# Kernel tuning notes

Hardware: AMD Instinct MI355X
Metric: run time of the kernel (lower is better)

## Reference

```python
import math
import jax, jax.numpy as jnp
import numpy as np

B, T, D = 4, 1024, 1024
H = 16
HD = D // H       # head_dim
DE = 64           # d_event
NT = 8            # n_event_types
NR = 64           # n_rules
NH = 4            # n_hits
NA = 2            # n_alternatives
SQ = math.sqrt(HD)


def setup_inputs() -> dict:
    key = jax.random.key(0)
    ks = jax.random.split(key, 16)
    s = 0.02
    f = jnp.float32
    return {
        "x": jax.random.normal(ks[0], (B, T, D), f),
        "W_node": jax.random.normal(ks[1], (D, D), f) * s,
        "W_value": jax.random.normal(ks[2], (D, D), f) * s,
        "W_out": jax.random.normal(ks[3], (D, D), f) * s,
        "arity_w": jax.random.normal(ks[4], (H, HD), f) * s,   # arity=3 -> one extra axis weight
        "W_event": jax.random.normal(ks[5], (D, DE), f) * s,
        "W_type": jax.random.normal(ks[6], (D, NT), f) * s,
        "patterns": jax.random.normal(ks[7], (NR, DE), f) * s,
        "W_actions": jax.random.normal(ks[8], (NA, D, D), f) * s,
        "W_alt": jax.random.normal(ks[9], (DE, NA), f) * s,
        "log_temp": jnp.zeros((), f),
        "Wg1": jax.random.normal(ks[10], (2 * D + 1, D), f) * s,
        "bg1": jnp.zeros((D,), f),
        "Wg2": jax.random.normal(ks[11], (D, 1), f) * s,
        "bg2": jnp.zeros((1,), f),
    }


def reference(x, W_node, W_value, W_out, arity_w, W_event, W_type, patterns,
              W_actions, W_alt, log_temp, Wg1, bg1, Wg2, bg2):
    # --- IsotropicAttention (arity=3, eval mode so dropout is identity) ---
    nodes = (x @ W_node).reshape(B, T, H, HD).transpose(0, 2, 1, 3)    # (B,H,T,HD)
    values = (x @ W_value).reshape(B, T, H, HD).transpose(0, 2, 1, 3)  # (B,H,T,HD)
    scores = jnp.einsum('bhtd,bhsd->bhts', nodes, nodes)
    scores = (scores + scores.transpose(0, 1, 3, 2)) * (0.5 / SQ)      # symmetrize + scale
    ax = jnp.einsum('bhtd,hd->bht', nodes, arity_w)                    # ternary axis score
    mod = jax.nn.sigmoid((ax[:, :, :, None] + ax[:, :, None, :]) / SQ)
    scores = scores * mod
    attn = jax.nn.softmax(scores, axis=-1)
    attn_out = jnp.einsum('bhts,bhsd->bthd', attn, values).reshape(B, T, D) @ W_out
    x1 = x + attn_out
    # --- EventGenerator ---
    events = x1 @ W_event                                              # (B,T,DE)
    event_types = jax.nn.softmax(x1 @ W_type, axis=-1)                 # (B,T,NT)
    # --- RuleBank: soft top-k hit activation ---
    en = events / jnp.maximum(jnp.linalg.norm(events, axis=-1, keepdims=True), 1e-12)
    pn = patterns / jnp.maximum(jnp.linalg.norm(patterns, axis=-1, keepdims=True), 1e-12)
    sim = en @ pn.T                                                    # (B,T,NR)
    topk_vals, topk_idx = jax.lax.top_k(sim, NH)
    temp = jnp.clip(jnp.exp(log_temp), 0.01, 10.0)
    hit_w = jax.nn.softmax(topk_vals / temp, axis=-1)                  # (B,T,NH)
    hit_patterns = patterns[topk_idx]                                  # (B,T,NH,DE)
    weighted_pattern = jnp.einsum('btkd,btk->btd', hit_patterns, hit_w)
    alt_w = jax.nn.softmax((weighted_pattern @ W_alt) / temp, axis=-1) # (B,T,NA)
    acted = jnp.einsum('btd,ade->btae', x1, W_actions)                 # (B,T,NA,D)
    actions_out = jnp.einsum('btae,bta->bte', acted, alt_w)
    hit_strength = jnp.max(topk_vals, axis=-1, keepdims=True)
    actions_out = actions_out * jax.nn.sigmoid(hit_strength)
    # --- TransactionGate: soft commit/rollback ---
    entropy = -jnp.sum(event_types * jnp.log(event_types + 1e-10), axis=-1, keepdims=True)
    entropy_norm = entropy / math.log(NT)
    gin = jnp.concatenate([x1, actions_out, entropy_norm], axis=-1)    # (B,T,2D+1)
    g = jax.nn.sigmoid(jax.nn.silu(gin @ Wg1 + bg1) @ Wg2 + bg2)       # (B,T,1)
    return x1 + g * actions_out
```

## Files before the change

kernel.cpp:

```cpp
#include <hip/hip_runtime.h>
#include <hip/hip_bf16.h>
#include <math.h>

#define B_  4
#define T_  1024
#define D_  1024
#define H_  16
#define HD_ 64
#define DE_ 64
#define NT_ 8
#define NR_ 64
#define NH_ 4

typedef __attribute__((ext_vector_type(8))) short short8;
typedef __attribute__((ext_vector_type(4))) short short4v;
typedef __attribute__((ext_vector_type(2))) unsigned uint2v;
typedef __attribute__((ext_vector_type(4))) float f4;

typedef __attribute__((address_space(1))) const unsigned int guint;
typedef __attribute__((address_space(3))) unsigned int suint;

__device__ __forceinline__ short f2bf(float f) {
    unsigned x = __float_as_uint(f);
    unsigned r = (x + 0x7fffu + ((x >> 16) & 1u)) >> 16;
    return (short)r;
}
__device__ __forceinline__ float bf2f(short s) {
    return __uint_as_float(((unsigned)(unsigned short)s) << 16);
}

__device__ __forceinline__ int swz64(int row, int slot) {
    return row * 64 + ((slot ^ (row & 7)) << 3);
}

__global__ __launch_bounds__(256) void castx_k(
    const float* __restrict__ x, short* __restrict__ xb)
{
    size_t i = ((size_t)blockIdx.x * 256 + threadIdx.x) * 8;
    float4 v0 = *(const float4*)&x[i];
    float4 v1 = *(const float4*)&x[i + 4];
    short8 o;
    o[0] = f2bf(v0.x); o[1] = f2bf(v0.y); o[2] = f2bf(v0.z); o[3] = f2bf(v0.w);
    o[4] = f2bf(v1.x); o[5] = f2bf(v1.y); o[6] = f2bf(v1.z); o[7] = f2bf(v1.w);
    *(short8*)&xb[i] = o;
}

struct TJ { const float* src; short* dst; int K, N, rs, ro, base; };
struct TJobs { TJ j[7]; };

__global__ __launch_bounds__(256) void tcast_all(TJobs jb)
{
    int bid = blockIdx.x;
    int ji = 0;
#pragma unroll
    for (int i = 1; i < 7; i++) if (bid >= jb.j[i].base) ji = i;
    const float* src = jb.j[ji].src;
    short* dst = jb.j[ji].dst;
    const int K = jb.j[ji].K, N = jb.j[ji].N;
    const int rs = jb.j[ji].rs, ro = jb.j[ji].ro;
    int rel = bid - jb.j[ji].base;
    int tiles_n = N >> 6;
    int k0 = (rel / tiles_n) * 64, n0 = (rel % tiles_n) * 64;

    __shared__ float tile[64][65];
    const int tid = threadIdx.x;
    const int r = tid >> 4, c = (tid & 15) * 4;
#pragma unroll
    for (int rep = 0; rep < 4; rep++) {
        int rr = rep * 16 + r;
        float4 v = *(const float4*)&src[(size_t)(k0 + rr) * N + n0 + c];
        tile[rr][c] = v.x; tile[rr][c + 1] = v.y; tile[rr][c + 2] = v.z; tile[rr][c + 3] = v.w;
    }
    __syncthreads();
#pragma unroll
    for (int rep = 0; rep < 4; rep++) {
        int n = rep * 16 + r;
        short4v p;
        p[0] = f2bf(tile[c + 0][n]);
        p[1] = f2bf(tile[c + 1][n]);
        p[2] = f2bf(tile[c + 2][n]);
        p[3] = f2bf(tile[c + 3][n]);
        *(short4v*)&dst[(size_t)((n0 + n) * rs + ro) * K + k0 + c] = p;
    }
}

__global__ __launch_bounds__(256) void ttype_k(
    const float* __restrict__ Wt, short* __restrict__ BTe)
{
    int idx = blockIdx.x * 256 + threadIdx.x;
    int n = idx >> 10, k = idx & 1023;
    BTe[(size_t)(64 + n) * 1024 + k] = f2bf(Wt[k * 8 + n]);
}

template<int AM>
__global__ __launch_bounds__(256) void gemm4(
    const short* __restrict__ A1, const short* __restrict__ A2, int Ks,
    const short* __restrict__ BT,
    float* __restrict__ C, short* __restrict__ Cb1, short* __restrict__ Cb2,
    int M, int N, int K, int epi,
    const float* __restrict__ resid, const float* __restrict__ ent,
    const float* __restrict__ w1e, const float* __restrict__ bias,
    const float* __restrict__ altw, const float* __restrict__ hitsig)
{
    constexpr int BM = AM * 32;
    constexpr int AR = (AM == 4) ? 2 : 4;
    constexpr int ANV = 64 / AR / 8;
    __shared__ short As[BM * 72];
    __shared__ short Bs[128 * 72];
    const int tid = threadIdx.x, wave = tid >> 6, lane = tid & 63;
    const int lrow = lane & 15, lq = lane >> 4;
    int bid = blockIdx.x;
    int tiles_m = M / BM;
    int mpx = tiles_m >> 3;
    int xcd = bid & 7, idx = bid >> 3;
    int mt = xcd * mpx + (idx % mpx);
    int nt = idx / mpx;
    const int m0 = mt * BM, n0 = nt * 128;
    const int wm = (wave >> 1) * (AM * 16), wn = (wave & 1) * 64;
    const int K2 = K - Ks;
    const int arow = tid / AR, ash = (tid % AR) * (64 / AR);
    const int brow = tid >> 1, bsh = (tid & 1) * 32;

    short8 va[ANV], vb[4];
    auto loadA = [&](int k0) {
        int ka = k0 + ash;
        const short* ap = (ka < Ks)
            ? A1 + (size_t)(m0 + arow) * Ks + ka
            : A2 + (size_t)(m0 + arow) * K2 + (ka - Ks);
#pragma unroll
        for (int u = 0; u < ANV; u++) va[u] = *(const short8*)(ap + u * 8);
    };
    auto loadB = [&](int k0) {
        const short* bp = BT + (size_t)(n0 + brow) * K + k0 + bsh;
#pragma unroll
        for (int u = 0; u < 4; u++) vb[u] = *(const short8*)(bp + u * 8);
    };

    loadA(0); loadB(0);
    f4 acc[AM][4] = {};

    for (int k0 = 0; k0 < K; k0 += 64) {
        __syncthreads();
#pragma unroll
        for (int u = 0; u < ANV; u++)
            *(short8*)&As[arow * 72 + ash + u * 8] = va[u];
#pragma unroll
        for (int u = 0; u < 4; u++)
            *(short8*)&Bs[brow * 72 + bsh + u * 8] = vb[u];
        __syncthreads();
        if (k0 + 64 < K) { loadA(k0 + 64); loadB(k0 + 64); }
#pragma unroll
        for (int kh = 0; kh < 2; kh++) {
            short8 af[AM], bfv[4];
#pragma unroll
            for (int i = 0; i < AM; i++)
                af[i] = *(short8*)&As[(wm + i * 16 + lrow) * 72 + kh * 32 + lq * 8];
#pragma unroll
            for (int j = 0; j < 4; j++)
                bfv[j] = *(short8*)&Bs[(wn + j * 16 + lrow) * 72 + kh * 32 + lq * 8];
#pragma unroll
            for (int i = 0; i < AM; i++)
#pragma unroll
                for (int j = 0; j < 4; j++)
                    acc[i][j] = __builtin_amdgcn_mfma_f32_16x16x32_bf16(
                        af[i], bfv[j], acc[i][j], 0, 0, 0);
        }
    }

#pragma unroll
    for (int i = 0; i < AM; i++) {
#pragma unroll
        for (int r = 0; r < 4; r++) {
            int row = m0 + wm + i * 16 + lq * 4 + r;
            float w0 = 0.f, w1 = 0.f, hs = 0.f;
            if (epi == 5) { w0 = altw[row * 2]; w1 = altw[row * 2 + 1]; hs = hitsig[row]; }
#pragma unroll
            for (int j = 0; j < 4; j++) {
                int col = n0 + wn + j * 16 + lrow;
                float v = acc[i][j][r];
                if (epi == 0) {
                    C[(size_t)row * N + col] = v;
                } else if (epi == 1) {
                    v += resid[(size_t)row * N + col];
                    C[(size_t)row * N + col] = v;
                    Cb1[(size_t)row * N + col] = f2bf(v);
                } else if (epi == 2) {
                    if (col < 1024) Cb1[(size_t)row * 1024 + col] = f2bf(v);
                    else            Cb2[(size_t)row * 1024 + col - 1024] = f2bf(v);
                } else if (epi == 3) {
                    v += ent[row] * w1e[col] + bias[col];
                    float sv = v * __builtin_amdgcn_rcpf(1.f + __expf(-v));
                    Cb1[(size_t)row * N + col] = f2bf(sv);
                } else {
                    float other = __shfl_xor(v, 1);
                    if ((lane & 1) == 0) {
                        float cv = (w0 * v + w1 * other) * hs;
                        Cb1[(size_t)row * 1024 + (col >> 1)] = f2bf(cv);
                    }
                }
            }
        }
    }
}

template<int AM>
__global__ __launch_bounds__(256) void gemm7(
    const short* __restrict__ A1, const short* __restrict__ A2, int Ks,
    const short* __restrict__ BT,
    float* __restrict__ C, short* __restrict__ Cb1, short* __restrict__ Cb2,
    int M, int N, int K, int epi,
    const float* __restrict__ resid, const float* __restrict__ ent,
    const float* __restrict__ w1e, const float* __restrict__ bias,
    const float* __restrict__ altw, const float* __restrict__ hitsig)
{
    constexpr int BM = AM * 32;
    constexpr int AISS = BM / 32;
    __shared__ short As[2][BM * 64];
    __shared__ short Bs[2][128 * 64];
    const int tid = threadIdx.x, wave = tid >> 6, lane = tid & 63;
    const int lrow = lane & 15, lq = lane >> 4;
    int bid = blockIdx.x;
    int tiles_m = M / BM;
    int mpx = tiles_m >> 3;
    int xcd = bid & 7, idx = bid >> 3;
    int mt = xcd * mpx + (idx % mpx);
    int ntile = idx / mpx;
    const int m0 = mt * BM, n0 = ntile * 128;
    const int wm = (wave >> 1) * (AM * 16), wn = (wave & 1) * 64;
    const int K2 = K - Ks;

    const int l8 = lane >> 3;
    const int cs = ((lane & 7) ^ l8) << 3;

    auto stageA = [&](int k0, int bu) {
#pragma unroll
        for (int u = 0; u < AISS; u++) {
            int r = wave * (AISS * 8) + u * 8 + l8;
            int ka = k0 + cs;
            const short* gp = (ka < Ks)
                ? A1 + (size_t)(m0 + r) * Ks + ka
                : A2 + (size_t)(m0 + r) * K2 + (ka - Ks);
            short* lp = &As[bu][wave * (AISS * 512) + u * 512];
            __builtin_amdgcn_global_load_lds((guint*)gp, (suint*)lp, 16, 0, 0);
        }
    };
    auto stageB = [&](int k0, int bu) {
#pragma unroll
        for (int u = 0; u < 4; u++) {
            int r = wave * 32 + u * 8 + l8;
            const short* gp = BT + (size_t)(n0 + r) * K + k0 + cs;
            short* lp = &Bs[bu][wave * 2048 + u * 512];
            __builtin_amdgcn_global_load_lds((guint*)gp, (suint*)lp, 16, 0, 0);
        }
    };

    stageA(0, 0); stageB(0, 0);
    f4 acc[AM][4] = {};
    const int nsteps = K >> 6;

    for (int t = 0; t < nsteps; t++) {
        const int cur = t & 1;
        __syncthreads();
        if (t + 1 < nsteps) {
            stageA((t + 1) << 6, cur ^ 1);
            stageB((t + 1) << 6, cur ^ 1);
        }
#pragma unroll
        for (int kh = 0; kh < 2; kh++) {
            short8 af[AM], bfv[4];
#pragma unroll
            for (int i = 0; i < AM; i++)
                af[i] = *(short8*)&As[cur][swz64(wm + i * 16 + lrow, kh * 4 + lq)];
#pragma unroll
            for (int j = 0; j < 4; j++)
                bfv[j] = *(short8*)&Bs[cur][swz64(wn + j * 16 + lrow, kh * 4 + lq)];
#pragma unroll
            for (int i = 0; i < AM; i++)
#pragma unroll
                for (int j = 0; j < 4; j++)
                    acc[i][j] = __builtin_amdgcn_mfma_f32_16x16x32_bf16(
                        af[i], bfv[j], acc[i][j], 0, 0, 0);
        }
    }

#pragma unroll
    for (int i = 0; i < AM; i++) {
#pragma unroll
        for (int r = 0; r < 4; r++) {
            int row = m0 + wm + i * 16 + lq * 4 + r;
            float w0 = 0.f, w1 = 0.f, hs = 0.f;
            if (epi == 5) { w0 = altw[row * 2]; w1 = altw[row * 2 + 1]; hs = hitsig[row]; }
#pragma unroll
            for (int j = 0; j < 4; j++) {
                int col = n0 + wn + j * 16 + lrow;
                float v = acc[i][j][r];
                if (epi == 0) {
                    C[(size_t)row * N + col] = v;
                } else if (epi == 1) {
                    v += resid[(size_t)row * N + col];
                    C[(size_t)row * N + col] = v;
                    Cb1[(size_t)row * N + col] = f2bf(v);
                } else if (epi == 2) {
                    if (col < 1024) Cb1[(size_t)row * 1024 + col] = f2bf(v);
                    else            Cb2[(size_t)row * 1024 + col - 1024] = f2bf(v);
                } else if (epi == 3) {
                    v += ent[row] * w1e[col] + bias[col];
                    float sv = v * __builtin_amdgcn_rcpf(1.f + __expf(-v));
                    Cb1[(size_t)row * N + col] = f2bf(sv);
                } else {
                    float other = __shfl_xor(v, 1);
                    if ((lane & 1) == 0) {
                        float cv = (w0 * v + w1 * other) * hs;
                        Cb1[(size_t)row * 1024 + (col >> 1)] = f2bf(cv);
                    }
                }
            }
        }
    }
}

__global__ __launch_bounds__(256) void vtrans_k(
    const short* __restrict__ vb, short* __restrict__ vtg)
{
    const int b = blockIdx.z, h = blockIdx.y, t0 = blockIdx.x * 64;
    const int tid = threadIdx.x;
    __shared__ short tile[64 * 72];
    const int row = tid >> 2, c = (tid & 3) * 16;
    const short* p = vb + (size_t)(b * T_ + t0 + row) * D_ + h * 64 + c;
    *(short8*)&tile[row * 72 + c + 0] = *(const short8*)(p + 0);
    *(short8*)&tile[row * 72 + c + 8] = *(const short8*)(p + 8);
    __syncthreads();
    short8 o0, o1;
#pragma unroll
    for (int i = 0; i < 8; i++) o0[i] = tile[(c + i) * 72 + row];
#pragma unroll
    for (int i = 0; i < 8; i++) o1[i] = tile[(c + 8 + i) * 72 + row];
    short* q = vtg + (size_t)((b * H_ + h) * 64 + row) * T_ + t0 + c;
    *(short8*)(q + 0) = o0;
    *(short8*)(q + 8) = o1;
}

__global__ __launch_bounds__(256) void ax_k(
    const short* __restrict__ nodes_bf, const float* __restrict__ arity_w,
    float* __restrict__ ax)
{
    int idx = blockIdx.x * 256 + threadIdx.x;
    int t = idx & (T_ - 1);
    int h = (idx >> 10) & (H_ - 1);
    int b = idx >> 14;
    const short* np_ = nodes_bf + (((size_t)b * T_ + t) * H_ + h) * HD_;
    float s = 0.f;
#pragma unroll
    for (int d = 0; d < HD_; d += 8) {
        short8 n8 = *(const short8*)&np_[d];
#pragma unroll
        for (int q = 0; q < 8; q++) s += bf2f(n8[q]) * arity_w[h * HD_ + d + q];
    }
    ax[idx] = s;
}

__global__ __launch_bounds__(256) void attn8_k(
    const short* __restrict__ nodes_bf, const short* __restrict__ vtg,
    const float* __restrict__ ax, short* __restrict__ attnp)
{
    const int b = blockIdx.z, h = blockIdx.y, t0 = blockIdx.x * 64;
    const int tid = threadIdx.x;
    const int wave = tid >> 6, lane = tid & 63;
    const int lrow = lane & 15, lq = lane >> 4;
    const int wm = wave * 16;
    const int row = tid >> 2, c4 = tid & 3;

    __shared__ short Ns[64 * 64];
    __shared__ short Vt[64 * 64];
    __shared__ short Pm[64 * 64];

    const short* qp = nodes_bf + (size_t)(b * T_ + t0 + wm + lrow) * D_ + h * 64;
    const short8 bt0 = *(const short8*)(qp + lq * 8);
    const short8 bt1 = *(const short8*)(qp + 32 + lq * 8);
    const float at8 = ax[(size_t)(b * H_ + h) * T_ + t0 + wm + lrow] * 0.125f;

    const short* np0 = nodes_bf + (size_t)(b * T_ + row) * D_ + h * 64 + c4 * 16;
    const short* vp0 = vtg + (size_t)((b * H_ + h) * 64 + row) * T_ + c4 * 16;
    const float* axp_ = ax + (size_t)(b * H_ + h) * T_;

    short8 vn0, vn1, vv0, vv1;
    f4 axv[4];
    auto preload = [&](int s0) {
        const short* np = np0 + (size_t)s0 * D_;
        const short* vp = vp0 + s0;
        vn0 = *(const short8*)(np + 0);
        vn1 = *(const short8*)(np + 8);
        vv0 = *(const short8*)(vp + 0);
        vv1 = *(const short8*)(vp + 8);
#pragma unroll
        for (int j = 0; j < 4; j++)
            axv[j] = *(const f4*)&axp_[s0 + j * 16 + lq * 4];
    };

    preload(0);

    float l_reg = 0.f;
    f4 O[4] = {};
    f4 axc[4];

    for (int s0 = 0; s0 < T_; s0 += 64) {
        __syncthreads();
        *(short8*)&Ns[swz64(row, 2 * c4 + 0)] = vn0;
        *(short8*)&Ns[swz64(row, 2 * c4 + 1)] = vn1;
        *(short8*)&Vt[swz64(row, 2 * c4 + 0)] = vv0;
        *(short8*)&Vt[swz64(row, 2 * c4 + 1)] = vv1;
#pragma unroll
        for (int j = 0; j < 4; j++) axc[j] = axv[j];
        __syncthreads();
        if (s0 + 64 < T_) preload(s0 + 64);

        float psum = 0.f;
#pragma unroll
        for (int j = 0; j < 4; j++) {
            short8 a0 = *(short8*)&Ns[swz64(j * 16 + lrow, lq)];
            short8 a1 = *(short8*)&Ns[swz64(j * 16 + lrow, 4 + lq)];
            f4 s = {0.f, 0.f, 0.f, 0.f};
            s = __builtin_amdgcn_mfma_f32_16x16x32_bf16(a0, bt0, s, 0, 0, 0);
            s = __builtin_amdgcn_mfma_f32_16x16x32_bf16(a1, bt1, s, 0, 0, 0);
            float p0, p1, p2, p3;
            {
                float z, zz, t1, mK;
                z = fmaf(axc[j][0], 0.125f, at8); zz = z * z;
                t1 = fmaf(zz, -0.0037570183f, 0.04508422f);
                mK = fmaf(z, t1, 0.09016844f);
                p0 = __builtin_amdgcn_exp2f(s[0] * mK);
                z = fmaf(axc[j][1], 0.125f, at8); zz = z * z;
                t1 = fmaf(zz, -0.0037570183f, 0.04508422f);
                mK = fmaf(z, t1, 0.09016844f);
                p1 = __builtin_amdgcn_exp2f(s[1] * mK);
                z = fmaf(axc[j][2], 0.125f, at8); zz = z * z;
                t1 = fmaf(zz, -0.0037570183f, 0.04508422f);
                mK = fmaf(z, t1, 0.09016844f);
                p2 = __builtin_amdgcn_exp2f(s[2] * mK);
                z = fmaf(axc[j][3], 0.125f, at8); zz = z * z;
                t1 = fmaf(zz, -0.0037570183f, 0.04508422f);
                mK = fmaf(z, t1, 0.09016844f);
                p3 = __builtin_amdgcn_exp2f(s[3] * mK);
            }
            psum += (p0 + p1) + (p2 + p3);
            unsigned u0, u1;
            asm("v_cvt_pk_bf16_f32 %0, %1, %2" : "=v"(u0) : "v"(p0), "v"(p1));
            asm("v_cvt_pk_bf16_f32 %0, %1, %2" : "=v"(u1) : "v"(p2), "v"(p3));
            uint2v uu; uu[0] = u0; uu[1] = u1;
            *(uint2v*)&Pm[swz64(wm + lrow, 2 * j + (lq >> 1)) + (lq & 1) * 4] = uu;
        }
        l_reg += psum;

        short8 pa0 = *(short8*)&Pm[swz64(wm + lrow, lq)];
        short8 pa1 = *(short8*)&Pm[swz64(wm + lrow, 4 + lq)];
#pragma unroll
        for (int dj = 0; dj < 4; dj++) {
            short8 v0 = *(short8*)&Vt[swz64(dj * 16 + lrow, lq)];
            short8 v1 = *(short8*)&Vt[swz64(dj * 16 + lrow, 4 + lq)];
            O[dj] = __builtin_amdgcn_mfma_f32_16x16x32_bf16(pa0, v0, O[dj], 0, 0, 0);
            O[dj] = __builtin_amdgcn_mfma_f32_16x16x32_bf16(pa1, v1, O[dj], 0, 0, 0);
        }
    }

    l_reg += __shfl_xor(l_reg, 16);
    l_reg += __shfl_xor(l_reg, 32);

    float linv[4];
#pragma unroll
    for (int r = 0; r < 4; r++)
        linv[r] = __builtin_amdgcn_rcpf(__shfl(l_reg, lq * 4 + r));
#pragma unroll
    for (int dj = 0; dj < 4; dj++)
#pragma unroll
        for (int r = 0; r < 4; r++)
            attnp[(size_t)(b * T_ + t0 + wm + lq * 4 + r) * D_ + h * 64 + dj * 16 + lrow] =
                f2bf(O[dj][r] * linv[r]);
}

__global__ __launch_bounds__(64) void pnorm_k(
    const float* __restrict__ patterns, float* __restrict__ pn)
{
    int r = blockIdx.x, lane = threadIdx.x;
    float v = patterns[r * 64 + lane];
    float ss = v * v;
    for (int off = 1; off < 64; off <<= 1) ss += __shfl_xor(ss, off);
    pn[r * 64 + lane] = v / fmaxf(sqrtf(ss), 1e-12f);
}

__global__ __launch_bounds__(256) void token2_k(
    const float* __restrict__ evlg, const float* __restrict__ pn,
    const float* __restrict__ patterns, const float* __restrict__ W_alt,
    const float* __restrict__ log_temp,
    float* __restrict__ entn, float* __restrict__ altw, float* __restrict__ hitsig)
{
    const int tid = threadIdx.x, wave = tid >> 6, lane = tid & 63;
    __shared__ float pn_sh[64 * 68];
    __shared__ float pat_sh[64 * 68];
    __shared__ float en_sh[4][68];
    {
        int row = tid >> 2, c = (tid & 3) * 16;
#pragma unroll
        for (int u = 0; u < 4; u++) {
            *(float4*)&pn_sh[row * 68 + c + u * 4]  = *(const float4*)&pn[row * 64 + c + u * 4];
            *(float4*)&pat_sh[row * 68 + c + u * 4] = *(const float4*)&patterns[row * 64 + c + u * 4];
        }
    }
    float temp = expf(log_temp[0]);
    temp = fminf(fmaxf(temp, 0.01f), 10.f);
    const float tinv = 1.f / temp;
    __syncthreads();

#pragma unroll
    for (int rep = 0; rep < 2; rep++) {
        const int m = blockIdx.x * 8 + wave * 2 + rep;
        float ev = evlg[(size_t)m * 128 + lane];
        float ss = ev * ev;
        for (int off = 1; off < 64; off <<= 1) ss += __shfl_xor(ss, off);
        float en = ev * __builtin_amdgcn_rcpf(fmaxf(sqrtf(ss), 1e-12f));
        en_sh[wave][lane] = en;
        float entv;
        {
            float lgt = evlg[(size_t)m * 128 + 64 + (lane & 7)];
            float mx = lgt;
            for (int off = 1; off < 8; off <<= 1) mx = fmaxf(mx, __shfl_xor(mx, off));
            float p = __expf(lgt - mx);
            float sum = p;
            for (int off = 1; off < 8; off <<= 1) sum += __shfl_xor(sum, off);
            float pi = p / sum;
            float term = -pi * __logf(pi + 1e-10f);
            float e = term;
            for (int off = 1; off < 8; off <<= 1) e += __shfl_xor(e, off);
            entv = e * 0.4808983f;
        }
        float sim = 0.f;
#pragma unroll
        for (int u = 0; u < 16; u++) {
            float4 e4 = *(float4*)&en_sh[wave][u * 4];
            float4 p4 = *(float4*)&pn_sh[lane * 68 + u * 4];
            sim += e4.x * p4.x + e4.y * p4.y + e4.z * p4.z + e4.w * p4.w;
        }
        float v = sim;
        float tv[NH_]; int tix[NH_];
#pragma unroll
        for (int kk = 0; kk < NH_; kk++) {
            float mv = v; int mi = lane;
            if (v == -1e30f) mi = 127;
            for (int off = 1; off < 64; off <<= 1) {
                float ov = __shfl_xor(mv, off);
                int   oi = __shfl_xor(mi, off);
                if (ov > mv || (ov == mv && oi < mi)) { mv = ov; mi = oi; }
            }
            tv[kk] = mv; tix[kk] = mi;
            if (lane == mi) v = -1e30f;
        }
        float hmx = tv[0];
        float hw[NH_], hsum = 0.f;
#pragma unroll
        for (int kk = 0; kk < NH_; kk++) { hw[kk] = __expf((tv[kk] - hmx) * tinv); hsum += hw[kk]; }
        float hsr = __builtin_amdgcn_rcpf(hsum);
        float wp = 0.f;
#pragma unroll
        for (int kk = 0; kk < NH_; kk++) wp += hw[kk] * hsr * pat_sh[tix[kk] * 68 + lane];
        float a0 = wp * W_alt[lane * 2 + 0];
        float a1 = wp * W_alt[lane * 2 + 1];
        for (int off = 1; off < 64; off <<= 1) {
            a0 += __shfl_xor(a0, off);
            a1 += __shfl_xor(a1, off);
        }
        a0 *= tinv; a1 *= tinv;
        float amx = fmaxf(a0, a1);
        float e0 = __expf(a0 - amx), e1 = __expf(a1 - amx);
        if (lane == 0) {
            float zr = __builtin_amdgcn_rcpf(e0 + e1);
            altw[m * 2 + 0] = e0 * zr;
            altw[m * 2 + 1] = e1 * zr;
            hitsig[m] = __builtin_amdgcn_rcpf(1.f + __expf(-tv[0]));
            entn[m] = entv;
        }
    }
}

__global__ __launch_bounds__(256) void gate_k(
    const short* __restrict__ h1_bf, const float* __restrict__ Wg2,
    const float* __restrict__ bg2, const float* __restrict__ x1,
    const short* __restrict__ actions_bf, float* __restrict__ out)
{
    const int m = blockIdx.x, tid = threadIdx.x;
    float part = 0.f;
    for (int d = tid; d < D_; d += 256)
        part += bf2f(h1_bf[(size_t)m * D_ + d]) * Wg2[d];
    __shared__ float red[256];
    red[tid] = part;
    __syncthreads();
    for (int w = 128; w > 0; w >>= 1) {
        if (tid < w) red[tid] += red[tid + w];
        __syncthreads();
    }
    float g = 1.f / (1.f + expf(-(red[0] + bg2[0])));
    for (int d = tid; d < D_; d += 256) {
        size_t i = (size_t)m * D_ + d;
        out[i] = x1[i] + g * bf2f(actions_bf[i]);
    }
}

extern "C" void kernel_launch(void* const* d_in, const int* in_sizes, int n_in,
                              void* d_out, int out_size, void* d_ws, size_t ws_size,
                              hipStream_t stream)
{
    const float* x        = (const float*)d_in[0];
    const float* W_node   = (const float*)d_in[1];
    const float* W_value  = (const float*)d_in[2];
    const float* W_out    = (const float*)d_in[3];
    const float* arity_w  = (const float*)d_in[4];
    const float* W_event  = (const float*)d_in[5];
    const float* W_type   = (const float*)d_in[6];
    const float* patterns = (const float*)d_in[7];
    const float* W_act    = (const float*)d_in[8];
    const float* W_alt    = (const float*)d_in[9];
    const float* log_temp = (const float*)d_in[10];
    const float* Wg1      = (const float*)d_in[11];
    const float* bg1      = (const float*)d_in[12];
    const float* Wg2      = (const float*)d_in[13];
    const float* bg2      = (const float*)d_in[14];
    float* out = (float*)d_out;

    const int M = B_ * T_;
    float* x1     = (float*)d_ws;
    float* evlg   = x1 + 4194304;
    float* axp    = evlg + 524288;
    float* pn     = axp + 65536;
    float* entn   = pn + 4096;
    float* altw   = entn + 4096;
    float* hitsig = altw + 8192;
    short* big       = (short*)(hitsig + 4096);
    short* xbf       = big;
    short* nodes_bf  = big + 1 * 4194304;
    short* values_bf = big + 2 * 4194304;
    short* vtg       = big + 3 * 4194304;
    short* x1_bf     = big + 4 * 4194304;
    short* wts       = big + 5 * 4194304;
    short* WnvT  = wts;
    short* WoT   = wts + 2 * 1048576;
    short* WaT   = wts + 3 * 1048576;
    short* Wg1T  = wts + 5 * 1048576;
    short* BTe   = wts + 7 * 1048576;
    short* actions_bf = vtg;
    short* h1_bf      = xbf;

    dim3 blk(256);
    dim3 g_bh(T_ / 64, H_, B_);

    castx_k<<<2048, blk, 0, stream>>>(x, xbf);
    pnorm_k<<<NR_, 64, 0, stream>>>(patterns, pn);
    TJobs jb;
    jb.j[0] = {W_node,            WnvT,           1024, 1024, 1, 0,    0};
    jb.j[1] = {W_value,           WnvT + 1048576, 1024, 1024, 1, 0,  256};
    jb.j[2] = {W_out,             WoT,            1024, 1024, 1, 0,  512};
    jb.j[3] = {W_act,             WaT,            1024, 1024, 2, 0,  768};
    jb.j[4] = {W_act + 1048576,   WaT,            1024, 1024, 2, 1, 1024};
    jb.j[5] = {Wg1,               Wg1T,           2048, 1024, 1, 0, 1280};
    jb.j[6] = {W_event,           BTe,            1024,   64, 1, 0, 1792};
    tcast_all<<<1808, blk, 0, stream>>>(jb);
    ttype_k<<<32, blk, 0, stream>>>(W_type, BTe);

    gemm7<4><<<512, blk, 0, stream>>>(xbf, xbf, D_, WnvT,
        nullptr, nodes_bf, values_bf, M, 2048, D_, 2,
        nullptr, nullptr, nullptr, nullptr, nullptr, nullptr);
    ax_k<<<256, blk, 0, stream>>>(nodes_bf, arity_w, axp);
    vtrans_k<<<g_bh, blk, 0, stream>>>(values_bf, vtg);
    attn8_k<<<g_bh, blk, 0, stream>>>(nodes_bf, vtg, axp, xbf);
    gemm4<2><<<512, blk, 0, stream>>>(xbf, xbf, D_, WoT,
        x1, x1_bf, nullptr, M, D_, D_, 1,
        x, nullptr, nullptr, nullptr, nullptr, nullptr);
    gemm4<2><<<64, blk, 0, stream>>>(x1_bf, x1_bf, D_, BTe,
        evlg, nullptr, nullptr, M, 128, D_, 0,
        nullptr, nullptr, nullptr, nullptr, nullptr, nullptr);
    token2_k<<<M / 8, blk, 0, stream>>>(evlg, pn, patterns, W_alt, log_temp,
                                        entn, altw, hitsig);
    gemm4<4><<<512, blk, 0, stream>>>(x1_bf, x1_bf, D_, WaT,
        nullptr, actions_bf, nullptr, M, 2048, D_, 5,
        nullptr, nullptr, nullptr, nullptr, altw, hitsig);
    gemm4<2><<<512, blk, 0, stream>>>(x1_bf, actions_bf, D_, Wg1T,
        nullptr, h1_bf, nullptr, M, D_, 2048, 3,
        nullptr, entn, Wg1 + (size_t)2048 * D_, bg1, nullptr, nullptr);
    gate_k<<<M, blk, 0, stream>>>(h1_bf, Wg2, bg2, x1, actions_bf, out);
}
```

Measured before the change: 342.5 us.

## Replace async LDS-DMA GEMM with register-staged padded-LDS kernel using 64-wide N tiles

Rewrites the GEMM kernel to stage tiles through registers into a single padded LDS buffer (row stride 72), in place of direct global-to-LDS loads into double-buffered swizzled tiles. It also halves the N tile to 64 and doubles the grid. The prefetch of the next K step into registers is meant to overlap memory with MFMA while cutting LDS use, and the smaller tiles give more blocks for occupancy. In exchange, each tile gets less reuse of the A operand, every step needs two barriers, and more global traffic is spent re-reading A. Four of the GEMM launches, formerly using gemm7 and gemm4, now use the new kernel; the epi==5 path is dropped from it.

```diff
diff --git a/kernel.cpp b/kernel.cpp
--- a/kernel.cpp
+++ b/kernel.cpp
@@ -16,9 +16,6 @@
 typedef __attribute__((ext_vector_type(4))) short short4v;
 typedef __attribute__((ext_vector_type(2))) unsigned uint2v;
 typedef __attribute__((ext_vector_type(4))) float f4;
-
-typedef __attribute__((address_space(1))) const unsigned int guint;
-typedef __attribute__((address_space(3))) unsigned int suint;
 
 __device__ __forceinline__ short f2bf(float f) {
     unsigned x = __float_as_uint(f);
@@ -204,7 +201,7 @@
 }
 
 template<int AM>
-__global__ __launch_bounds__(256) void gemm7(
+__global__ __launch_bounds__(256) void gemm8(
     const short* __restrict__ A1, const short* __restrict__ A2, int Ks,
     const short* __restrict__ BT,
     float* __restrict__ C, short* __restrict__ Cb1, short* __restrict__ Cb2,
@@ -214,9 +211,10 @@
     const float* __restrict__ altw, const float* __restrict__ hitsig)
 {
     constexpr int BM = AM * 32;
-    constexpr int AISS = BM / 32;
-    __shared__ short As[2][BM * 64];
-    __shared__ short Bs[2][128 * 64];
+    constexpr int AR = (AM == 4) ? 2 : 4;
+    constexpr int ANV = 64 / AR / 8;
+    __shared__ short As[BM * 72];
+    __shared__ short Bs[64 * 72];
     const int tid = threadIdx.x, wave = tid >> 6, lane = tid & 63;
     const int lrow = lane & 15, lq = lane >> 4;
     int bid = blockIdx.x;
@@ -224,60 +222,54 @@
     int mpx = tiles_m >> 3;
     int xcd = bid & 7, idx = bid >> 3;
     int mt = xcd * mpx + (idx % mpx);
-    int ntile = idx / mpx;
-    const int m0 = mt * BM, n0 = ntile * 128;
-    const int wm = (wave >> 1) * (AM * 16), wn = (wave & 1) * 64;
+    int nt = idx / mpx;
+    const int m0 = mt * BM, n0 = nt * 64;
+    const int wm = (wave >> 1) * (AM * 16), wn = (wave & 1) * 32;
     const int K2 = K - Ks;
-
-    const int l8 = lane >> 3;
-    const int cs = ((lane & 7) ^ l8) << 3;
-
-    auto stageA = [&](int k0, int bu) {
-#pragma unroll
-        for (int u = 0; u < AISS; u++) {
-            int r = wave * (AISS * 8) + u * 8 + l8;
-            int ka = k0 + cs;
-            const short* gp = (ka < Ks)
-                ? A1 + (size_t)(m0 + r) * Ks + ka
-                : A2 + (size_t)(m0 + r) * K2 + (ka - Ks);
-            short* lp = &As[bu][wave * (AISS * 512) + u * 512];
-            __builtin_amdgcn_global_load_lds((guint*)gp, (suint*)lp, 16, 0, 0);
-        }
+    const int arow = tid / AR, ash = (tid % AR) * (64 / AR);
+    const int brow = tid >> 2, bsh = (tid & 3) * 16;
+
+    short8 va[ANV], vb[2];
+    auto loadA = [&](int k0) {
+        int ka = k0 + ash;
+        const short* ap = (ka < Ks)
+            ? A1 + (size_t)(m0 + arow) * Ks + ka
+            : A2 + (size_t)(m0 + arow) * K2 + (ka - Ks);
+#pragma unroll
+        for (int u = 0; u < ANV; u++) va[u] = *(const short8*)(ap + u * 8);
     };
-    auto stageB = [&](int k0, int bu) {
-#pragma unroll
-        for (int u = 0; u < 4; u++) {
-            int r = wave * 32 + u * 8 + l8;
-            const short* gp = BT + (size_t)(n0 + r) * K + k0 + cs;
-            short* lp = &Bs[bu][wave * 2048 + u * 512];
-            __builtin_amdgcn_global_load_lds((guint*)gp, (suint*)lp, 16, 0, 0);
-        }
+    auto loadB = [&](int k0) {
+        const short* bp = BT + (size_t)(n0 + brow) * K + k0 + bsh;
+#pragma unroll
+        for (int u = 0; u < 2; u++) vb[u] = *(const short8*)(bp + u * 8);
     };
 
-    stageA(0, 0); stageB(0, 0);
-    f4 acc[AM][4] = {};
-    const int nsteps = K >> 6;
-
-    for (int t = 0; t < nsteps; t++) {
-        const int cur = t & 1;
+    loadA(0); loadB(0);
+    f4 acc[AM][2] = {};
+
+    for (int k0 = 0; k0 < K; k0 += 64) {
         __syncthreads();
-        if (t + 1 < nsteps) {
-            stageA((t + 1) << 6, cur ^ 1);
-            stageB((t + 1) << 6, cur ^ 1);
-        }
+#pragma unroll
+        for (int u = 0; u < ANV; u++)
+            *(short8*)&As[arow * 72 + ash + u * 8] = va[u];
+#pragma unroll
+        for (int u = 0; u < 2; u++)
+            *(short8*)&Bs[brow * 72 + bsh + u * 8] = vb[u];
+        __syncthreads();
+        if (k0 + 64 < K) { loadA(k0 + 64); loadB(k0 + 64); }
 #pragma unroll
         for (int kh = 0; kh < 2; kh++) {
-            short8 af[AM], bfv[4];
+            short8 af[AM], bfv[2];
 #pragma unroll
             for (int i = 0; i < AM; i++)
-                af[i] = *(short8*)&As[cur][swz64(wm + i * 16 + lrow, kh * 4 + lq)];
-#pragma unroll
-            for (int j = 0; j < 4; j++)
-                bfv[j] = *(short8*)&Bs[cur][swz64(wn + j * 16 + lrow, kh * 4 + lq)];
+                af[i] = *(short8*)&As[(wm + i * 16 + lrow) * 72 + kh * 32 + lq * 8];
+#pragma unroll
+            for (int j = 0; j < 2; j++)
+                bfv[j] = *(short8*)&Bs[(wn + j * 16 + lrow) * 72 + kh * 32 + lq * 8];
 #pragma unroll
             for (int i = 0; i < AM; i++)
 #pragma unroll
-                for (int j = 0; j < 4; j++)
+                for (int j = 0; j < 2; j++)
                     acc[i][j] = __builtin_amdgcn_mfma_f32_16x16x32_bf16(
                         af[i], bfv[j], acc[i][j], 0, 0, 0);
         }
@@ -288,10 +280,8 @@
 #pragma unroll
         for (int r = 0; r < 4; r++) {
             int row = m0 + wm + i * 16 + lq * 4 + r;
-            float w0 = 0.f, w1 = 0.f, hs = 0.f;
-            if (epi == 5) { w0 = altw[row * 2]; w1 = altw[row * 2 + 1]; hs = hitsig[row]; }
-#pragma unroll
-            for (int j = 0; j < 4; j++) {
+#pragma unroll
+            for (int j = 0; j < 2; j++) {
                 int col = n0 + wn + j * 16 + lrow;
                 float v = acc[i][j][r];
                 if (epi == 0) {
@@ -307,12 +297,6 @@
                     v += ent[row] * w1e[col] + bias[col];
                     float sv = v * __builtin_amdgcn_rcpf(1.f + __expf(-v));
                     Cb1[(size_t)row * N + col] = f2bf(sv);
-                } else {
-                    float other = __shfl_xor(v, 1);
-                    if ((lane & 1) == 0) {
-                        float cv = (w0 * v + w1 * other) * hs;
-                        Cb1[(size_t)row * 1024 + (col >> 1)] = f2bf(cv);
-                    }
                 }
             }
         }
@@ -663,16 +647,16 @@
     tcast_all<<<1808, blk, 0, stream>>>(jb);
     ttype_k<<<32, blk, 0, stream>>>(W_type, BTe);
 
-    gemm7<4><<<512, blk, 0, stream>>>(xbf, xbf, D_, WnvT,
+    gemm8<4><<<1024, blk, 0, stream>>>(xbf, xbf, D_, WnvT,
         nullptr, nodes_bf, values_bf, M, 2048, D_, 2,
         nullptr, nullptr, nullptr, nullptr, nullptr, nullptr);
     ax_k<<<256, blk, 0, stream>>>(nodes_bf, arity_w, axp);
     vtrans_k<<<g_bh, blk, 0, stream>>>(values_bf, vtg);
     attn8_k<<<g_bh, blk, 0, stream>>>(nodes_bf, vtg, axp, xbf);
-    gemm4<2><<<512, blk, 0, stream>>>(xbf, xbf, D_, WoT,
+    gemm8<2><<<1024, blk, 0, stream>>>(xbf, xbf, D_, WoT,
         x1, x1_bf, nullptr, M, D_, D_, 1,
         x, nullptr, nullptr, nullptr, nullptr, nullptr);
-    gemm4<2><<<64, blk, 0, stream>>>(x1_bf, x1_bf, D_, BTe,
+    gemm8<2><<<128, blk, 0, stream>>>(x1_bf, x1_bf, D_, BTe,
         evlg, nullptr, nullptr, M, 128, D_, 0,
         nullptr, nullptr, nullptr, nullptr, nullptr, nullptr);
     token2_k<<<M / 8, blk, 0, stream>>>(evlg, pn, patterns, W_alt, log_temp,
@@ -680,7 +664,7 @@
     gemm4<4><<<512, blk, 0, stream>>>(x1_bf, x1_bf, D_, WaT,
         nullptr, actions_bf, nullptr, M, 2048, D_, 5,
         nullptr, nullptr, nullptr, nullptr, altw, hitsig);
-    gemm4<2><<<512, blk, 0, stream>>>(x1_bf, actions_bf, D_, Wg1T,
+    gemm8<2><<<1024, blk, 0, stream>>>(x1_bf, actions_bf, D_, Wg1T,
         nullptr, h1_bf, nullptr, M, D_, 2048, 3,
         nullptr, entn, Wg1 + (size_t)2048 * D_, bg1, nullptr, nullptr);
     gate_k<<<M, blk, 0, stream>>>(h1_bf, Wg2, bg2, x1, actions_bf, out);
```

New measurement: 322.8 us. 1.06x faster.
